# Optimization experiments

Hardware: AMD Instinct MI355X
Metric: run time of the kernel (lower is better)

Reference implementation:

```python
import jax, jax.numpy as jnp
import numpy as np

B, D, P, K, L_S = 512, 1024, 64, 16, 16


def _make_M():
    # fixed signed mask: top-left PxP block = -1, bottom-left KxP block = +1
    M = np.zeros((P + K, P + K), dtype=np.float32)
    M[:P, :P] = -1.0
    M[P:, :P] = +1.0
    return jnp.asarray(M)


def setup_inputs() -> dict:
    key = jax.random.key(0)
    k1, k2, k3 = jax.random.split(key, 3)
    X_tilde = jax.random.normal(k1, (B, D, P + K), dtype=jnp.float32)
    y_train = jax.random.normal(k2, (B, P), dtype=jnp.float32)
    gamma = jax.random.normal(k3, (D,), dtype=jnp.float32) * 0.01
    return {"X_tilde": X_tilde, "y_train": y_train, "gamma": gamma}


def reference(X_tilde, y_train, gamma):
    M = _make_M()  # [P+K, P+K]
    Bsz = X_tilde.shape[0]
    # h0 = [y_train, 0_K]  -> [B, P+K]
    h0 = jnp.concatenate([y_train, jnp.zeros((Bsz, K), dtype=y_train.dtype)], axis=-1)
    # score[b,m,n] = sum_d gamma[d] * X[b,d,m] * X[b,d,n] / P
    weighted = gamma[None, :, None] * X_tilde  # [B, D, P+K]
    score = jnp.einsum('bdm,bdn->bmn', weighted, X_tilde) / float(P)
    masked_score = M[None, :, :] * score  # [B, P+K, P+K]
    inv_L = 1.0 / float(L_S)

    def step(h, _):
        h = h + inv_L * jnp.einsum('bmn,bn->bm', masked_score, h)
        return h, None

    h, _ = jax.lax.scan(step, h0, None, length=L_S)
    return h[:, P:]
```

## Files before the change

kernel.cpp:

```cpp
#include <hip/hip_runtime.h>


namespace {
typedef __attribute__((ext_vector_type(8))) short bf16x8;
typedef __attribute__((ext_vector_type(4))) float f32x4;
typedef __attribute__((ext_vector_type(4))) float fv4;
typedef __attribute__((ext_vector_type(2))) unsigned uv2;

constexpr int kB  = 512;
constexpr int kD  = 1024;
constexpr int kP  = 64;
constexpr int kKK = 16;
constexpr int kLS = 16;
constexpr int kThreads = 640;
constexpr int kKc = 64;
constexpr int kNC = kD / kKc;

constexpr int TB    = 4096;
constexpr int ASZ   = 80 * 128;
constexpr int BSZ   = 64 * 128;
constexpr int BUFSZ = ASZ + BSZ;
constexpr int LDS_BYTES = TB + 2 * BUFSZ;

__device__ __forceinline__ unsigned short bf16_bits(float x) {
  unsigned u = __builtin_bit_cast(unsigned, x);
  u += 0x7fffu + ((u >> 16) & 1u);
  return (unsigned short)(u >> 16);
}
__device__ __forceinline__ unsigned bpack(float lo, float hi) {
  return (unsigned)bf16_bits(lo) | ((unsigned)bf16_bits(hi) << 16);
}
__device__ __forceinline__ int fswz(int r) {
  return ((r & 7) ^ ((r >> 2) & 7)) << 4;
}

__device__ __forceinline__ void stage_chunk(char* __restrict__ Ab, char* __restrict__ Bb,
                                            int ct, int kt,
                                            const fv4& v0, const fv4& v1,
                                            const fv4& v2, const fv4& v3,
                                            const fv4& g4) {
#pragma unroll
  for (int j = 0; j < 4; ++j) {
    const int m = 4 * ct + j;
    const int off = m * 128 + ((8 * kt) ^ fswz(m));
    uv2 wa; wa.x = bpack(v0[j], v1[j]); wa.y = bpack(v2[j], v3[j]);
    *reinterpret_cast<uv2*>(Ab + off) = wa;
    if (ct < 16) {
      uv2 wb; wb.x = bpack(g4[0] * v0[j], g4[1] * v1[j]);
      wb.y = bpack(g4[2] * v2[j], g4[3] * v3[j]);
      *reinterpret_cast<uv2*>(Bb + off) = wb;
    }
  }
}

__global__ void __launch_bounds__(kThreads)
tcsf_kernel(const float* __restrict__ X, const float* __restrict__ y,
            const float* __restrict__ gamma, float* __restrict__ out) {
  __shared__ __align__(16) char smem[LDS_BYTES];
  float* gs = reinterpret_cast<float*>(smem);

  const int t = threadIdx.x;
  const int b = blockIdx.x;
  const int l = t & 63;
  const int w = t >> 6;
  const int grp = (w >= 5) ? 1 : 0;
  const int slab = grp ? (w - 5) : w;
  const int tg = grp ? (t - 320) : t;
  const int ct = tg % 20;
  const int kt = tg / 20;

  float yv = 0.f;
  if (t < kP) yv = y[b * kP + t];
  for (int i = t; i < kD; i += kThreads) gs[i] = gamma[i];

  const fv4* Xg = reinterpret_cast<const fv4*>(X) + (size_t)b * (kD * 80 / 4);

  f32x4 acc[4];
#pragma unroll
  for (int nt = 0; nt < 4; ++nt) acc[nt] = (f32x4)(0.f);

  fv4 v0, v1, v2, v3;

  {
    const int base = (grp * kKc + 4 * kt) * 20 + ct;
    v0 = Xg[base]; v1 = Xg[base + 20]; v2 = Xg[base + 40]; v3 = Xg[base + 60];
  }
  __syncthreads();
  if (!grp) {
    const fv4 g4 = *reinterpret_cast<const fv4*>(gs + 4 * kt);
    stage_chunk(smem + TB, smem + TB + ASZ, ct, kt, v0, v1, v2, v3, g4);
    const int base = (2 * kKc + 4 * kt) * 20 + ct;
    v0 = Xg[base]; v1 = Xg[base + 20]; v2 = Xg[base + 40]; v3 = Xg[base + 60];
  }
  __syncthreads();

  const int rA = 16 * slab + (l & 15);
  const int cbb = grp * 64 + (l >> 4) * 16;
  const int offA = rA * 128 + (cbb ^ fswz(rA));
  int offB[4];
#pragma unroll
  for (int nt = 0; nt < 4; ++nt) {
    const int rB = 16 * nt + (l & 15);
    offB[nt] = rB * 128 + (cbb ^ fswz(rB));
  }

  for (int c = 0; c < kNC; ++c) {
    if (grp == ((c + 1) & 1)) {
      if (c + 1 < kNC) {
        const fv4 g4 = *reinterpret_cast<const fv4*>(gs + (c + 1) * kKc + 4 * kt);
        char* Ab = smem + TB + ((c + 1) & 1) * BUFSZ;
        stage_chunk(Ab, Ab + ASZ, ct, kt, v0, v1, v2, v3, g4);
      }
      if (c + 3 < kNC) {
        const int base = ((c + 3) * kKc + 4 * kt) * 20 + ct;
        v0 = Xg[base]; v1 = Xg[base + 20]; v2 = Xg[base + 40]; v3 = Xg[base + 60];
      }
    }
    const char* Ab = smem + TB + (c & 1) * BUFSZ;
    const char* Bb = Ab + ASZ;
    const bf16x8 a = *reinterpret_cast<const bf16x8*>(Ab + offA);
#pragma unroll
    for (int nt = 0; nt < 4; ++nt) {
      const bf16x8 bb = *reinterpret_cast<const bf16x8*>(Bb + offB[nt]);
      acc[nt] = __builtin_amdgcn_mfma_f32_16x16x32_bf16(a, bb, acc[nt], 0, 0, 0);
    }
    __syncthreads();
  }

  float* Gl = reinterpret_cast<float*>(smem + TB);
  float* hp = Gl + 80 * 65;
  constexpr float invP = 1.0f / 64.0f;
  if (grp) {
#pragma unroll
    for (int nt = 0; nt < 4; ++nt)
#pragma unroll
      for (int r = 0; r < 4; ++r)
        Gl[(16 * slab + (l >> 4) * 4 + r) * 65 + 16 * nt + (l & 15)] = acc[nt][r];
  }
  __syncthreads();
  if (!grp) {
#pragma unroll
    for (int nt = 0; nt < 4; ++nt)
#pragma unroll
      for (int r = 0; r < 4; ++r) {
        const int idx = (16 * slab + (l >> 4) * 4 + r) * 65 + 16 * nt + (l & 15);
        Gl[idx] = (Gl[idx] + acc[nt][r]) * invP;
      }
  }
  if (t < kP) hp[t] = yv;
  __syncthreads();

  const int m = t >> 3;
  const int part = t & 7;
  const float* Grow = Gl + m * 65 + part * 8;
  float hk = 0.f;
  constexpr float invL = 1.0f / kLS;
  for (int s = 0; s < kLS; ++s) {
    const float* hpc = hp + (s & 1) * kP;
    const float* hpp = hpc + part * 8;
    float d0 = 0.f, d1 = 0.f, d2 = 0.f, d3 = 0.f;
#pragma unroll
    for (int i = 0; i < 8; i += 4) {
      d0 = fmaf(Grow[i + 0], hpp[i + 0], d0);
      d1 = fmaf(Grow[i + 1], hpp[i + 1], d1);
      d2 = fmaf(Grow[i + 2], hpp[i + 2], d2);
      d3 = fmaf(Grow[i + 3], hpp[i + 3], d3);
    }
    float dot = (d0 + d1) + (d2 + d3);
    dot += __shfl_xor(dot, 1);
    dot += __shfl_xor(dot, 2);
    dot += __shfl_xor(dot, 4);
    if (part == 0) {
      if (m < kP) hp[((s + 1) & 1) * kP + m] = hpc[m] - invL * dot;
      else        hk += invL * dot;
    }
    __syncthreads();
  }
  if (part == 0 && m >= kP) out[b * kKK + (m - kP)] = hk;
}

}

extern "C" void kernel_launch(void* const* d_in, const int* in_sizes, int n_in,
                              void* d_out, int out_size, void* d_ws, size_t ws_size,
                              hipStream_t stream) {
  const float* X     = (const float*)d_in[0];
  const float* y     = (const float*)d_in[1];
  const float* gamma = (const float*)d_in[2];
  float* out = (float*)d_out;
  tcsf_kernel<<<dim3(kB), dim3(kThreads), 0, stream>>>(X, y, gamma, out);
}
```

Measured before the change: 41.06 us.

## Split block into dedicated producer and MFMA consumer warps

Replaces the two alternating groups that both staged and computed with a warp-specialized design. Five producer waves load X from global, convert to bf16 and stage into LDS. Three consumer waves run the MFMAs over the full K=128 of each chunk, holding one or two 16-row fragments each, so the cross-group accumulator reduction through LDS disappears. The block drops from 640 to 512 threads with a 4-blocks launch bound to raise occupancy. The prefetch depth shrinks, and the recurrence switches to 4 threads per row with an extra barrier per step, which may add latency.

```diff
diff --git a/kernel.cpp b/kernel.cpp
--- a/kernel.cpp
+++ b/kernel.cpp
@@ -10,9 +10,10 @@
 constexpr int kB  = 512;
 constexpr int kD  = 1024;
 constexpr int kP  = 64;
+constexpr int kPK = 80;
 constexpr int kKK = 16;
 constexpr int kLS = 16;
-constexpr int kThreads = 640;
+constexpr int kThreads = 512;
 constexpr int kKc = 64;
 constexpr int kNC = kD / kKc;
 
@@ -53,7 +54,7 @@
   }
 }
 
-__global__ void __launch_bounds__(kThreads)
+__global__ void __launch_bounds__(kThreads, 4)
 tcsf_kernel(const float* __restrict__ X, const float* __restrict__ y,
             const float* __restrict__ gamma, float* __restrict__ out) {
   __shared__ __align__(16) char smem[LDS_BYTES];
@@ -63,11 +64,7 @@
   const int b = blockIdx.x;
   const int l = t & 63;
   const int w = t >> 6;
-  const int grp = (w >= 5) ? 1 : 0;
-  const int slab = grp ? (w - 5) : w;
-  const int tg = grp ? (t - 320) : t;
-  const int ct = tg % 20;
-  const int kt = tg / 20;
+  const bool producer = (w >= 3);
 
   float yv = 0.f;
   if (t < kP) yv = y[b * kP + t];
@@ -75,54 +72,77 @@
 
   const fv4* Xg = reinterpret_cast<const fv4*>(X) + (size_t)b * (kD * 80 / 4);
 
-  f32x4 acc[4];
-#pragma unroll
-  for (int nt = 0; nt < 4; ++nt) acc[nt] = (f32x4)(0.f);
-
+  int ct = 0, kt = 0;
   fv4 v0, v1, v2, v3;
-
-  {
-    const int base = (grp * kKc + 4 * kt) * 20 + ct;
+  if (producer) {
+    const int tg = t - 192;
+    ct = tg % 20;
+    kt = tg / 20;
+    const int base = (4 * kt) * 20 + ct;
     v0 = Xg[base]; v1 = Xg[base + 20]; v2 = Xg[base + 40]; v3 = Xg[base + 60];
   }
+
+  f32x4 acc[2][4];
+#pragma unroll
+  for (int f = 0; f < 2; ++f)
+#pragma unroll
+    for (int nt = 0; nt < 4; ++nt) acc[f][nt] = (f32x4)(0.f);
+  int offA[2][2], offB[4][2];
+  if (!producer) {
+    const int lane15 = l & 15, kq = l >> 4;
+    const int r00 = 32 * w;
+#pragma unroll
+    for (int f = 0; f < 2; ++f) {
+      const int r = r00 + 16 * f + lane15;
+#pragma unroll
+      for (int ks = 0; ks < 2; ++ks)
+        offA[f][ks] = r * 128 + ((ks * 64 + kq * 16) ^ fswz(r));
+    }
+#pragma unroll
+    for (int nt = 0; nt < 4; ++nt) {
+      const int r = 16 * nt + lane15;
+#pragma unroll
+      for (int ks = 0; ks < 2; ++ks)
+        offB[nt][ks] = r * 128 + ((ks * 64 + kq * 16) ^ fswz(r));
+    }
+  }
+
   __syncthreads();
-  if (!grp) {
+  if (producer) {
     const fv4 g4 = *reinterpret_cast<const fv4*>(gs + 4 * kt);
     stage_chunk(smem + TB, smem + TB + ASZ, ct, kt, v0, v1, v2, v3, g4);
-    const int base = (2 * kKc + 4 * kt) * 20 + ct;
+    const int base = (kKc + 4 * kt) * 20 + ct;
     v0 = Xg[base]; v1 = Xg[base + 20]; v2 = Xg[base + 40]; v3 = Xg[base + 60];
   }
   __syncthreads();
 
-  const int rA = 16 * slab + (l & 15);
-  const int cbb = grp * 64 + (l >> 4) * 16;
-  const int offA = rA * 128 + (cbb ^ fswz(rA));
-  int offB[4];
-#pragma unroll
-  for (int nt = 0; nt < 4; ++nt) {
-    const int rB = 16 * nt + (l & 15);
-    offB[nt] = rB * 128 + (cbb ^ fswz(rB));
-  }
-
   for (int c = 0; c < kNC; ++c) {
-    if (grp == ((c + 1) & 1)) {
+    if (producer) {
       if (c + 1 < kNC) {
         const fv4 g4 = *reinterpret_cast<const fv4*>(gs + (c + 1) * kKc + 4 * kt);
         char* Ab = smem + TB + ((c + 1) & 1) * BUFSZ;
         stage_chunk(Ab, Ab + ASZ, ct, kt, v0, v1, v2, v3, g4);
       }
-      if (c + 3 < kNC) {
-        const int base = ((c + 3) * kKc + 4 * kt) * 20 + ct;
+      if (c + 2 < kNC) {
+        const int base = ((c + 2) * kKc + 4 * kt) * 20 + ct;
         v0 = Xg[base]; v1 = Xg[base + 20]; v2 = Xg[base + 40]; v3 = Xg[base + 60];
       }
-    }
-    const char* Ab = smem + TB + (c & 1) * BUFSZ;
-    const char* Bb = Ab + ASZ;
-    const bf16x8 a = *reinterpret_cast<const bf16x8*>(Ab + offA);
-#pragma unroll
-    for (int nt = 0; nt < 4; ++nt) {
-      const bf16x8 bb = *reinterpret_cast<const bf16x8*>(Bb + offB[nt]);
-      acc[nt] = __builtin_amdgcn_mfma_f32_16x16x32_bf16(a, bb, acc[nt], 0, 0, 0);
+    } else {
+      const char* Ab = smem + TB + (c & 1) * BUFSZ;
+      const char* Bb = Ab + ASZ;
+#pragma unroll
+      for (int ks = 0; ks < 2; ++ks) {
+        const bf16x8 a0 = *reinterpret_cast<const bf16x8*>(Ab + offA[0][ks]);
+        bf16x8 a1 = a0;
+        if (w < 2) a1 = *reinterpret_cast<const bf16x8*>(Ab + offA[1][ks]);
+#pragma unroll
+        for (int nt = 0; nt < 4; ++nt) {
+          const bf16x8 bb = *reinterpret_cast<const bf16x8*>(Bb + offB[nt][ks]);
+          acc[0][nt] = __builtin_amdgcn_mfma_f32_16x16x32_bf16(a0, bb, acc[0][nt], 0, 0, 0);
+          if (w < 2)
+            acc[1][nt] = __builtin_amdgcn_mfma_f32_16x16x32_bf16(a1, bb, acc[1][nt], 0, 0, 0);
+        }
+      }
     }
     __syncthreads();
   }
@@ -130,53 +150,50 @@
   float* Gl = reinterpret_cast<float*>(smem + TB);
   float* hp = Gl + 80 * 65;
   constexpr float invP = 1.0f / 64.0f;
-  if (grp) {
-#pragma unroll
-    for (int nt = 0; nt < 4; ++nt)
-#pragma unroll
-      for (int r = 0; r < 4; ++r)
-        Gl[(16 * slab + (l >> 4) * 4 + r) * 65 + 16 * nt + (l & 15)] = acc[nt][r];
-  }
-  __syncthreads();
-  if (!grp) {
-#pragma unroll
-    for (int nt = 0; nt < 4; ++nt)
-#pragma unroll
-      for (int r = 0; r < 4; ++r) {
-        const int idx = (16 * slab + (l >> 4) * 4 + r) * 65 + 16 * nt + (l & 15);
-        Gl[idx] = (Gl[idx] + acc[nt][r]) * invP;
-      }
+  if (!producer) {
+    const int lane15 = l & 15, kq = l >> 4;
+    const int nf = (w < 2) ? 2 : 1;
+    for (int f = 0; f < nf; ++f)
+#pragma unroll
+      for (int nt = 0; nt < 4; ++nt)
+#pragma unroll
+        for (int r = 0; r < 4; ++r)
+          Gl[(32 * w + 16 * f + kq * 4 + r) * 65 + 16 * nt + lane15] =
+              acc[f][nt][r] * invP;
   }
   if (t < kP) hp[t] = yv;
   __syncthreads();
 
-  const int m = t >> 3;
-  const int part = t & 7;
-  const float* Grow = Gl + m * 65 + part * 8;
+  const int m = t >> 2;
+  const int part = t & 3;
+  const bool act = (m < kPK);
+  const float* Grow = Gl + m * 65 + part * 16;
+  const float* hpp = hp + part * 16;
   float hk = 0.f;
   constexpr float invL = 1.0f / kLS;
   for (int s = 0; s < kLS; ++s) {
-    const float* hpc = hp + (s & 1) * kP;
-    const float* hpp = hpc + part * 8;
-    float d0 = 0.f, d1 = 0.f, d2 = 0.f, d3 = 0.f;
-#pragma unroll
-    for (int i = 0; i < 8; i += 4) {
-      d0 = fmaf(Grow[i + 0], hpp[i + 0], d0);
-      d1 = fmaf(Grow[i + 1], hpp[i + 1], d1);
-      d2 = fmaf(Grow[i + 2], hpp[i + 2], d2);
-      d3 = fmaf(Grow[i + 3], hpp[i + 3], d3);
-    }
-    float dot = (d0 + d1) + (d2 + d3);
-    dot += __shfl_xor(dot, 1);
-    dot += __shfl_xor(dot, 2);
-    dot += __shfl_xor(dot, 4);
-    if (part == 0) {
-      if (m < kP) hp[((s + 1) & 1) * kP + m] = hpc[m] - invL * dot;
-      else        hk += invL * dot;
+    float dot = 0.f;
+    if (act) {
+      float d0 = 0.f, d1 = 0.f, d2 = 0.f, d3 = 0.f;
+#pragma unroll
+      for (int i = 0; i < 16; i += 4) {
+        d0 = fmaf(Grow[i + 0], hpp[i + 0], d0);
+        d1 = fmaf(Grow[i + 1], hpp[i + 1], d1);
+        d2 = fmaf(Grow[i + 2], hpp[i + 2], d2);
+        d3 = fmaf(Grow[i + 3], hpp[i + 3], d3);
+      }
+      dot = (d0 + d1) + (d2 + d3);
+      dot += __shfl_xor(dot, 1);
+      dot += __shfl_xor(dot, 2);
     }
     __syncthreads();
-  }
-  if (part == 0 && m >= kP) out[b * kKK + (m - kP)] = hk;
+    if (act && part == 0) {
+      if (m < kP) hp[m] -= invL * dot;
+      else        hk   += invL * dot;
+    }
+    __syncthreads();
+  }
+  if (act && part == 0 && m >= kP) out[b * kKK + (m - kP)] = hk;
 }
 
 }
```

Result: faster. 40.22 us (-2.0%).
